# Kernel tuning notes

Measured on AMD Instinct MI355X. Metric: run time of the kernel, lower is better.

The kernel has to match this reference:

```python
import jax, jax.numpy as jnp
import numpy as np

B, N, D = 16, 4096, 128          # graphs, points per graph, feature dim
RATIO = 0.25
M = int(N * RATIO)               # 1024 sampled points per graph (static)
RADIUS = 0.2


def setup_inputs() -> dict:
    key = jax.random.key(0)
    k1, k2 = jax.random.split(key)
    x = jax.random.normal(k1, (B * N, D), dtype=jnp.float32)
    pos = jax.random.uniform(k2, (B * N, 3), dtype=jnp.float32)  # unit cube
    batch = jnp.repeat(jnp.arange(B, dtype=jnp.int32), N)        # sorted, equal-size graphs
    return {"x": x, "pos": pos, "batch": batch}


def _fps(pos_g):
    """Farthest point sampling on one graph. pos_g: [N,3] -> [M] int indices.
    Deterministic start at index 0 (random_start=False, i.e. eval mode)."""
    def step(carry, _):
        dist, last = carry
        d = jnp.sum((pos_g - pos_g[last]) ** 2, axis=-1)   # [N]
        dist = jnp.minimum(dist, d)                        # dist to nearest selected
        nxt = jnp.argmax(dist).astype(jnp.int32)
        return (dist, nxt), last
    init = (jnp.full((pos_g.shape[0],), jnp.inf, pos_g.dtype), jnp.int32(0))
    _, idx = jax.lax.scan(step, init, None, length=M)
    return idx  # [M]


def reference(x, pos, batch):
    # Equal-size graphs -> reshape instead of segment bookkeeping.
    pos_b = pos.reshape(B, N, 3)
    x_b = x.reshape(B, N, D)

    # FPS per graph, vmapped (sequential greedy selection inside lax.scan).
    idx = jax.vmap(_fps)(pos_b)                                    # [B, M]

    sampled_pos = jnp.take_along_axis(pos_b, idx[:, :, None], axis=1)  # [B, M, 3]
    sampled_x = jnp.take_along_axis(x_b, idx[:, :, None], axis=1)      # [B, M, D]

    # radius_graph within each graph: boolean adjacency (j within r of i, no self loops).
    diff = sampled_pos[:, :, None, :] - sampled_pos[:, None, :, :]     # [B, M, M, 3]
    d2 = jnp.sum(diff * diff, axis=-1)                                 # [B, M, M]
    adj = (d2 <= RADIUS * RADIUS) & ~jnp.eye(M, dtype=bool)[None]      # [B, M, M]

    sampled_batch = jnp.repeat(jnp.arange(B, dtype=batch.dtype), M)    # [B*M]
    return (sampled_x.reshape(B * M, D),
            sampled_pos.reshape(B * M, 3),
            sampled_batch,
            adj)
```

## Files before the change

kernel.cpp:

```cpp
#include <hip/hip_runtime.h>
#include <stdint.h>

#define BB 16
#define NN 4096
#define DD 128
#define MM 1024
#define RADIUS2 0.04f
#define TPB 256
#define PPT 16
#define NPAIR (PPT / 2)
#define NW 4

typedef unsigned long long u64;
typedef unsigned int u32;
typedef float f32x2 __attribute__((ext_vector_type(2)));
typedef unsigned int uint2v __attribute__((ext_vector_type(2)));

__device__ __forceinline__ u32 umin2(u32 a, u32 b) { return a < b ? a : b; }
__device__ __forceinline__ u32 umin3(u32 a, u32 b, u32 c) { return umin2(umin2(a, b), c); }
__device__ __forceinline__ float fmax3(float a, float b, float c) { return fmaxf(fmaxf(a, b), c); }

template <int CTRL>
__device__ __forceinline__ float dpp_fmax(float v) {
    int o = __builtin_amdgcn_update_dpp(0, __float_as_int(v), CTRL, 0xF, 0xF, true);
    return fmaxf(v, __int_as_float(o));
}
__device__ __forceinline__ float xor16_fmax(float v) {
#if __has_builtin(__builtin_amdgcn_permlane16_swap)
    uint2v r = __builtin_amdgcn_permlane16_swap(__float_as_uint(v), __float_as_uint(v), false, false);
    return fmaxf(__uint_as_float(r[0]), __uint_as_float(r[1]));
#else
    int o = __builtin_amdgcn_ds_swizzle(__float_as_int(v), 0x401F);
    return fmaxf(v, __int_as_float(o));
#endif
}
__device__ __forceinline__ float xor32_fmax(float v) {
#if __has_builtin(__builtin_amdgcn_permlane32_swap)
    uint2v r = __builtin_amdgcn_permlane32_swap(__float_as_uint(v), __float_as_uint(v), false, false);
    return fmaxf(__uint_as_float(r[0]), __uint_as_float(r[1]));
#else
    return fmaxf(v, __shfl_xor(v, 32, 64));
#endif
}
__device__ __forceinline__ float wave_fmax(float v) {
    v = dpp_fmax<0xB1>(v);
    v = dpp_fmax<0x4E>(v);
    v = dpp_fmax<0x141>(v);
    v = dpp_fmax<0x140>(v);
    v = xor16_fmax(v);
    v = xor32_fmax(v);
    return v;
}

__global__ __launch_bounds__(TPB) void fps_kernel(const float* __restrict__ pos,
                                                  int* __restrict__ idx_out) {
    const int b    = blockIdx.x;
    const int tid  = threadIdx.x;
    const int wid  = tid >> 6;
    const int lane = tid & 63;

    __shared__ float4 pos4[NN];
    __shared__ __align__(16) float4 cslot[2][NW];
    __shared__ __align__(16) u32    tslot[2][NW];
    __shared__ int trace[MM];

    const float* pg = pos + (size_t)b * NN * 3;
    for (int k = tid; k < NN * 3; k += TPB)
        ((float*)&pos4[k / 3])[k % 3] = pg[k];
    if (tid < 8) ((u32*)tslot)[tid] = 0;
    if (tid == 0) trace[0] = 0;
    __syncthreads();

    const int base = tid * PPT;
    f32x2 px[NPAIR], py[NPAIR], pz[NPAIR], dist2[NPAIR];
#pragma unroll
    for (int j = 0; j < NPAIR; ++j) {
        float4 a = pos4[base + 2 * j];
        float4 c = pos4[base + 2 * j + 1];
        px[j] = (f32x2){a.x, c.x};
        py[j] = (f32x2){a.y, c.y};
        pz[j] = (f32x2){a.z, c.z};
        dist2[j] = (f32x2){__builtin_inff(), __builtin_inff()};
    }

    float4 lp = pos4[0];
    float lx = lp.x, ly = lp.y, lz = lp.z;

    for (int m = 1; m < MM; ++m) {
        {
#pragma clang fp contract(off)
            f32x2 vx = {lx, lx}, vy = {ly, ly}, vz = {lz, lz};
#pragma unroll
            for (int j = 0; j < NPAIR; ++j) {
                f32x2 dx = px[j] - vx;
                f32x2 dy = py[j] - vy;
                f32x2 dz = pz[j] - vz;
                f32x2 d  = dx * dx + dy * dy;
                d = d + dz * dz;
                dist2[j] = __builtin_elementwise_min(dist2[j], d);
            }
        }

        float t0 = fmaxf(dist2[0].x, dist2[0].y);
        float t1 = fmaxf(dist2[1].x, dist2[1].y);
        float t2 = fmaxf(dist2[2].x, dist2[2].y);
        float t3 = fmaxf(dist2[3].x, dist2[3].y);
        float t4 = fmaxf(dist2[4].x, dist2[4].y);
        float t5 = fmaxf(dist2[5].x, dist2[5].y);
        float t6 = fmaxf(dist2[6].x, dist2[6].y);
        float t7 = fmaxf(dist2[7].x, dist2[7].y);
        float tmax = fmax3(fmax3(t0, t1, t2), fmax3(t3, t4, t5), fmaxf(t6, t7));

        u32 c[PPT];
#pragma unroll
        for (int j = 0; j < NPAIR; ++j) {
            c[2 * j]     = (dist2[j].x == tmax) ? (u32)(2 * j)     : 64u;
            c[2 * j + 1] = (dist2[j].y == tmax) ? (u32)(2 * j + 1) : 64u;
        }
        u32 a0 = umin3(c[0],  c[1],  c[2]);
        u32 a1 = umin3(c[3],  c[4],  c[5]);
        u32 a2 = umin3(c[6],  c[7],  c[8]);
        u32 a3 = umin3(c[9],  c[10], c[11]);
        u32 a4 = umin3(c[12], c[13], c[14]);
        u32 sl = umin3(umin3(a0, a1, a2), umin2(a3, a4), c[15]);
        u32 gidx = (u32)base + sl;

        float4 sp = pos4[gidx];

        float wmax = wave_fmax(tmax);

        u64 mk    = __ballot(tmax == wmax);
        int owner = (int)__builtin_ctzll(mk);

        const int buf = m & 1;
        const u32 tagm = (u32)m << 12;
        if (lane == owner) {
            cslot[buf][wid] = make_float4(sp.x, sp.y, sp.z, wmax);
            asm volatile("" ::: "memory");
            tslot[buf][wid] = tagm | gidx;
        }

        uint4 tg; float4 q0, q1, q2, q3;
        do {
            asm volatile("" ::: "memory");
            tg = *(const uint4*)&tslot[buf][0];
            q0 = cslot[buf][0];
            q1 = cslot[buf][1];
            q2 = cslot[buf][2];
            q3 = cslot[buf][3];
        } while ((((tg.x ^ tagm) | (tg.y ^ tagm) | (tg.z ^ tagm) | (tg.w ^ tagm))
                  & 0xFFFFF000u) != 0);

        float g = fmaxf(fmaxf(q0.w, q1.w), fmaxf(q2.w, q3.w));
        float nx = q3.x, ny = q3.y, nz = q3.z; u32 li = tg.w & 0xFFFu;
        bool s2 = (q2.w == g); nx = s2 ? q2.x : nx; ny = s2 ? q2.y : ny; nz = s2 ? q2.z : nz; li = s2 ? (tg.z & 0xFFFu) : li;
        bool s1 = (q1.w == g); nx = s1 ? q1.x : nx; ny = s1 ? q1.y : ny; nz = s1 ? q1.z : nz; li = s1 ? (tg.y & 0xFFFu) : li;
        bool s0 = (q0.w == g); nx = s0 ? q0.x : nx; ny = s0 ? q0.y : ny; nz = s0 ? q0.z : nz; li = s0 ? (tg.x & 0xFFFu) : li;
        lx = nx; ly = ny; lz = nz;

        if (tid == 0) trace[m] = (int)li;
    }

    __syncthreads();
    for (int k = tid; k < MM; k += TPB)
        idx_out[b * MM + k] = trace[k];
}

__global__ void gather_x_kernel(const float* __restrict__ x,
                                const int* __restrict__ idx,
                                float* __restrict__ out) {
    int t = blockIdx.x * blockDim.x + threadIdx.x;
    if (t >= BB * MM * DD / 4) return;
    int row = t >> 5;
    int c4  = (t & 31) << 2;
    int b   = row >> 10;
    int n   = idx[row];
    const float4 v = *(const float4*)(x + ((size_t)(b * NN + n) * DD + c4));
    *(float4*)(out + (size_t)row * DD + c4) = v;
}

__global__ void gather_pb_kernel(const float* __restrict__ pos,
                                 const int* __restrict__ idx,
                                 float* __restrict__ spos,
                                 float* __restrict__ sbatch) {
    int r = blockIdx.x * blockDim.x + threadIdx.x;
    if (r >= BB * MM) return;
    int b = r >> 10;
    int n = idx[r];
    const float* p = pos + (size_t)(b * NN + n) * 3;
    spos[r * 3 + 0] = p[0];
    spos[r * 3 + 1] = p[1];
    spos[r * 3 + 2] = p[2];
    sbatch[r] = (float)b;
}

__global__ void adj_kernel(const float* __restrict__ spos,
                           float* __restrict__ adj) {
    int row = blockIdx.x;
    int b   = row >> 10;
    int i   = row & (MM - 1);
    const float* pb = spos + (size_t)b * MM * 3;
    float xi = pb[i * 3 + 0];
    float yi = pb[i * 3 + 1];
    float zi = pb[i * 3 + 2];

    int j0 = threadIdx.x << 2;
    float4 r;
    float* o = adj + (size_t)row * MM;
#pragma unroll
    for (int k = 0; k < 4; ++k) {
        int j = j0 + k;
        float dx = xi - pb[j * 3 + 0];
        float dy = yi - pb[j * 3 + 1];
        float dz = zi - pb[j * 3 + 2];
        float d2 = __fadd_rn(__fadd_rn(__fmul_rn(dx, dx), __fmul_rn(dy, dy)),
                             __fmul_rn(dz, dz));
        float v = (d2 <= RADIUS2 && j != i) ? 1.0f : 0.0f;
        ((float*)&r)[k] = v;
    }
    *(float4*)(o + j0) = r;
}

extern "C" void kernel_launch(void* const* d_in, const int* in_sizes, int n_in,
                              void* d_out, int out_size, void* d_ws, size_t ws_size,
                              hipStream_t stream) {
    const float* x   = (const float*)d_in[0];
    const float* pos = (const float*)d_in[1];

    float* out    = (float*)d_out;
    int*   idx_ws = (int*)d_ws;

    float* sx   = out;
    float* spos = sx + (size_t)BB * MM * DD;
    float* sbat = spos + (size_t)BB * MM * 3;
    float* adj  = sbat + (size_t)BB * MM;

    fps_kernel<<<BB, TPB, 0, stream>>>(pos, idx_ws);
    gather_x_kernel<<<(BB * MM * DD / 4 + 255) / 256, 256, 0, stream>>>(x, idx_ws, sx);
    gather_pb_kernel<<<(BB * MM + 255) / 256, 256, 0, stream>>>(pos, idx_ws, spos, sbat);
    adj_kernel<<<BB * MM, 256, 0, stream>>>(spos, adj);
}
```

Baseline: 744.0 us.

## Process two graphs per FPS block and replace spin-wait with barrier

The FPS kernel now handles two graphs per workgroup, interleaving their distance updates and reductions so the independent dependency chains can hide each other's latency. It launches half as many blocks. The tag-polling spin loop on shared memory is replaced by a __syncthreads barrier per iteration. This doubles register use per thread and halves the number of concurrently active CUs, trading parallelism for instruction-level overlap.

```diff
diff --git a/kernel.cpp b/kernel.cpp
--- a/kernel.cpp
+++ b/kernel.cpp
@@ -54,116 +54,152 @@
 
 __global__ __launch_bounds__(TPB) void fps_kernel(const float* __restrict__ pos,
                                                   int* __restrict__ idx_out) {
-    const int b    = blockIdx.x;
     const int tid  = threadIdx.x;
     const int wid  = tid >> 6;
     const int lane = tid & 63;
-
-    __shared__ float4 pos4[NN];
-    __shared__ __align__(16) float4 cslot[2][NW];
-    __shared__ __align__(16) u32    tslot[2][NW];
-    __shared__ int trace[MM];
-
-    const float* pg = pos + (size_t)b * NN * 3;
-    for (int k = tid; k < NN * 3; k += TPB)
-        ((float*)&pos4[k / 3])[k % 3] = pg[k];
-    if (tid < 8) ((u32*)tslot)[tid] = 0;
-    if (tid == 0) trace[0] = 0;
+    const int gA   = blockIdx.x * 2;
+    const int gB   = gA + 1;
+
+    __shared__ float4 posA[NN], posB[NN];
+    __shared__ float4 fpart[2][2][NW];
+    __shared__ u32    ipart[2][2][NW];
+    __shared__ int    trace[2][MM];
+
+    const float* pga = pos + (size_t)gA * NN * 3;
+    const float* pgb = pos + (size_t)gB * NN * 3;
+    for (int k = tid; k < NN * 3; k += TPB) {
+        ((float*)&posA[k / 3])[k % 3] = pga[k];
+        ((float*)&posB[k / 3])[k % 3] = pgb[k];
+    }
+    if (tid == 0) { trace[0][0] = 0; trace[1][0] = 0; }
     __syncthreads();
 
     const int base = tid * PPT;
-    f32x2 px[NPAIR], py[NPAIR], pz[NPAIR], dist2[NPAIR];
+    f32x2 pxA[NPAIR], pyA[NPAIR], pzA[NPAIR], dA[NPAIR];
+    f32x2 pxB[NPAIR], pyB[NPAIR], pzB[NPAIR], dB[NPAIR];
 #pragma unroll
     for (int j = 0; j < NPAIR; ++j) {
-        float4 a = pos4[base + 2 * j];
-        float4 c = pos4[base + 2 * j + 1];
-        px[j] = (f32x2){a.x, c.x};
-        py[j] = (f32x2){a.y, c.y};
-        pz[j] = (f32x2){a.z, c.z};
-        dist2[j] = (f32x2){__builtin_inff(), __builtin_inff()};
-    }
-
-    float4 lp = pos4[0];
-    float lx = lp.x, ly = lp.y, lz = lp.z;
+        float4 a0 = posA[base + 2 * j], a1 = posA[base + 2 * j + 1];
+        pxA[j] = (f32x2){a0.x, a1.x}; pyA[j] = (f32x2){a0.y, a1.y}; pzA[j] = (f32x2){a0.z, a1.z};
+        dA[j] = (f32x2){__builtin_inff(), __builtin_inff()};
+        float4 b0 = posB[base + 2 * j], b1 = posB[base + 2 * j + 1];
+        pxB[j] = (f32x2){b0.x, b1.x}; pyB[j] = (f32x2){b0.y, b1.y}; pzB[j] = (f32x2){b0.z, b1.z};
+        dB[j] = (f32x2){__builtin_inff(), __builtin_inff()};
+    }
+
+    float4 lpA = posA[0], lpB = posB[0];
+    float lxa = lpA.x, lya = lpA.y, lza = lpA.z;
+    float lxb = lpB.x, lyb = lpB.y, lzb = lpB.z;
 
     for (int m = 1; m < MM; ++m) {
         {
 #pragma clang fp contract(off)
-            f32x2 vx = {lx, lx}, vy = {ly, ly}, vz = {lz, lz};
+            f32x2 vxa = {lxa, lxa}, vya = {lya, lya}, vza = {lza, lza};
+            f32x2 vxb = {lxb, lxb}, vyb = {lyb, lyb}, vzb = {lzb, lzb};
 #pragma unroll
             for (int j = 0; j < NPAIR; ++j) {
-                f32x2 dx = px[j] - vx;
-                f32x2 dy = py[j] - vy;
-                f32x2 dz = pz[j] - vz;
-                f32x2 d  = dx * dx + dy * dy;
-                d = d + dz * dz;
-                dist2[j] = __builtin_elementwise_min(dist2[j], d);
+                f32x2 dxa = pxA[j] - vxa, dya = pyA[j] - vya, dza = pzA[j] - vza;
+                f32x2 dxb = pxB[j] - vxb, dyb = pyB[j] - vyb, dzb = pzB[j] - vzb;
+                f32x2 da = dxa * dxa + dya * dya; da = da + dza * dza;
+                f32x2 db = dxb * dxb + dyb * dyb; db = db + dzb * dzb;
+                dA[j] = __builtin_elementwise_min(dA[j], da);
+                dB[j] = __builtin_elementwise_min(dB[j], db);
             }
         }
 
-        float t0 = fmaxf(dist2[0].x, dist2[0].y);
-        float t1 = fmaxf(dist2[1].x, dist2[1].y);
-        float t2 = fmaxf(dist2[2].x, dist2[2].y);
-        float t3 = fmaxf(dist2[3].x, dist2[3].y);
-        float t4 = fmaxf(dist2[4].x, dist2[4].y);
-        float t5 = fmaxf(dist2[5].x, dist2[5].y);
-        float t6 = fmaxf(dist2[6].x, dist2[6].y);
-        float t7 = fmaxf(dist2[7].x, dist2[7].y);
-        float tmax = fmax3(fmax3(t0, t1, t2), fmax3(t3, t4, t5), fmaxf(t6, t7));
-
-        u32 c[PPT];
+        float ta0 = fmaxf(dA[0].x, dA[0].y), ta1 = fmaxf(dA[1].x, dA[1].y);
+        float ta2 = fmaxf(dA[2].x, dA[2].y), ta3 = fmaxf(dA[3].x, dA[3].y);
+        float ta4 = fmaxf(dA[4].x, dA[4].y), ta5 = fmaxf(dA[5].x, dA[5].y);
+        float ta6 = fmaxf(dA[6].x, dA[6].y), ta7 = fmaxf(dA[7].x, dA[7].y);
+        float tmaxA = fmax3(fmax3(ta0, ta1, ta2), fmax3(ta3, ta4, ta5), fmaxf(ta6, ta7));
+        float tb0 = fmaxf(dB[0].x, dB[0].y), tb1 = fmaxf(dB[1].x, dB[1].y);
+        float tb2 = fmaxf(dB[2].x, dB[2].y), tb3 = fmaxf(dB[3].x, dB[3].y);
+        float tb4 = fmaxf(dB[4].x, dB[4].y), tb5 = fmaxf(dB[5].x, dB[5].y);
+        float tb6 = fmaxf(dB[6].x, dB[6].y), tb7 = fmaxf(dB[7].x, dB[7].y);
+        float tmaxB = fmax3(fmax3(tb0, tb1, tb2), fmax3(tb3, tb4, tb5), fmaxf(tb6, tb7));
+
+        u32 cA[PPT], cB[PPT];
 #pragma unroll
         for (int j = 0; j < NPAIR; ++j) {
-            c[2 * j]     = (dist2[j].x == tmax) ? (u32)(2 * j)     : 64u;
-            c[2 * j + 1] = (dist2[j].y == tmax) ? (u32)(2 * j + 1) : 64u;
-        }
-        u32 a0 = umin3(c[0],  c[1],  c[2]);
-        u32 a1 = umin3(c[3],  c[4],  c[5]);
-        u32 a2 = umin3(c[6],  c[7],  c[8]);
-        u32 a3 = umin3(c[9],  c[10], c[11]);
-        u32 a4 = umin3(c[12], c[13], c[14]);
-        u32 sl = umin3(umin3(a0, a1, a2), umin2(a3, a4), c[15]);
-        u32 gidx = (u32)base + sl;
-
-        float4 sp = pos4[gidx];
-
-        float wmax = wave_fmax(tmax);
-
-        u64 mk    = __ballot(tmax == wmax);
-        int owner = (int)__builtin_ctzll(mk);
+            cA[2 * j]     = (dA[j].x == tmaxA) ? (u32)(2 * j)     : 64u;
+            cA[2 * j + 1] = (dA[j].y == tmaxA) ? (u32)(2 * j + 1) : 64u;
+            cB[2 * j]     = (dB[j].x == tmaxB) ? (u32)(2 * j)     : 64u;
+            cB[2 * j + 1] = (dB[j].y == tmaxB) ? (u32)(2 * j + 1) : 64u;
+        }
+        u32 sA = umin3(umin3(umin3(cA[0], cA[1], cA[2]),  umin3(cA[3], cA[4], cA[5]),
+                             umin3(cA[6], cA[7], cA[8])),
+                       umin2(umin3(cA[9], cA[10], cA[11]), umin3(cA[12], cA[13], cA[14])),
+                       cA[15]);
+        u32 sB = umin3(umin3(umin3(cB[0], cB[1], cB[2]),  umin3(cB[3], cB[4], cB[5]),
+                             umin3(cB[6], cB[7], cB[8])),
+                       umin2(umin3(cB[9], cB[10], cB[11]), umin3(cB[12], cB[13], cB[14])),
+                       cB[15]);
+        u32 gidxA = (u32)base + sA;
+        u32 gidxB = (u32)base + sB;
+
+        float4 spA = posA[gidxA];
+        float4 spB = posB[gidxB];
+
+        float wmaxA = wave_fmax(tmaxA);
+        float wmaxB = wave_fmax(tmaxB);
+
+        u64 mkA = __ballot(tmaxA == wmaxA);
+        u64 mkB = __ballot(tmaxB == wmaxB);
+        int ownerA = (int)__builtin_ctzll(mkA);
+        int ownerB = (int)__builtin_ctzll(mkB);
 
         const int buf = m & 1;
-        const u32 tagm = (u32)m << 12;
-        if (lane == owner) {
-            cslot[buf][wid] = make_float4(sp.x, sp.y, sp.z, wmax);
-            asm volatile("" ::: "memory");
-            tslot[buf][wid] = tagm | gidx;
-        }
-
-        uint4 tg; float4 q0, q1, q2, q3;
-        do {
-            asm volatile("" ::: "memory");
-            tg = *(const uint4*)&tslot[buf][0];
-            q0 = cslot[buf][0];
-            q1 = cslot[buf][1];
-            q2 = cslot[buf][2];
-            q3 = cslot[buf][3];
-        } while ((((tg.x ^ tagm) | (tg.y ^ tagm) | (tg.z ^ tagm) | (tg.w ^ tagm))
-                  & 0xFFFFF000u) != 0);
-
-        float g = fmaxf(fmaxf(q0.w, q1.w), fmaxf(q2.w, q3.w));
-        float nx = q3.x, ny = q3.y, nz = q3.z; u32 li = tg.w & 0xFFFu;
-        bool s2 = (q2.w == g); nx = s2 ? q2.x : nx; ny = s2 ? q2.y : ny; nz = s2 ? q2.z : nz; li = s2 ? (tg.z & 0xFFFu) : li;
-        bool s1 = (q1.w == g); nx = s1 ? q1.x : nx; ny = s1 ? q1.y : ny; nz = s1 ? q1.z : nz; li = s1 ? (tg.y & 0xFFFu) : li;
-        bool s0 = (q0.w == g); nx = s0 ? q0.x : nx; ny = s0 ? q0.y : ny; nz = s0 ? q0.z : nz; li = s0 ? (tg.x & 0xFFFu) : li;
-        lx = nx; ly = ny; lz = nz;
-
-        if (tid == 0) trace[m] = (int)li;
+        if (lane == ownerA) {
+            fpart[0][buf][wid] = make_float4(wmaxA, spA.x, spA.y, spA.z);
+            ipart[0][buf][wid] = gidxA;
+        }
+        if (lane == ownerB) {
+            fpart[1][buf][wid] = make_float4(wmaxB, spB.x, spB.y, spB.z);
+            ipart[1][buf][wid] = gidxB;
+        }
+        __syncthreads();
+
+        {
+            float4 q0 = fpart[0][buf][0], q1 = fpart[0][buf][1];
+            float4 q2 = fpart[0][buf][2], q3 = fpart[0][buf][3];
+            float g = fmaxf(fmaxf(q0.x, q1.x), fmaxf(q2.x, q3.x));
+            float nx = q3.y, ny = q3.z, nz = q3.w;
+            bool s2 = (q2.x == g); nx = s2 ? q2.y : nx; ny = s2 ? q2.z : ny; nz = s2 ? q2.w : nz;
+            bool s1 = (q1.x == g); nx = s1 ? q1.y : nx; ny = s1 ? q1.z : ny; nz = s1 ? q1.w : nz;
+            bool s0 = (q0.x == g); nx = s0 ? q0.y : nx; ny = s0 ? q0.z : ny; nz = s0 ? q0.w : nz;
+            lxa = nx; lya = ny; lza = nz;
+            if (tid == 0) {
+                u32 li = ipart[0][buf][3];
+                li = s2 ? ipart[0][buf][2] : li;
+                li = s1 ? ipart[0][buf][1] : li;
+                li = s0 ? ipart[0][buf][0] : li;
+                trace[0][m] = (int)li;
+            }
+        }
+        {
+            float4 q0 = fpart[1][buf][0], q1 = fpart[1][buf][1];
+            float4 q2 = fpart[1][buf][2], q3 = fpart[1][buf][3];
+            float g = fmaxf(fmaxf(q0.x, q1.x), fmaxf(q2.x, q3.x));
+            float nx = q3.y, ny = q3.z, nz = q3.w;
+            bool s2 = (q2.x == g); nx = s2 ? q2.y : nx; ny = s2 ? q2.z : ny; nz = s2 ? q2.w : nz;
+            bool s1 = (q1.x == g); nx = s1 ? q1.y : nx; ny = s1 ? q1.z : ny; nz = s1 ? q1.w : nz;
+            bool s0 = (q0.x == g); nx = s0 ? q0.y : nx; ny = s0 ? q0.z : ny; nz = s0 ? q0.w : nz;
+            lxb = nx; lyb = ny; lzb = nz;
+            if (tid == 0) {
+                u32 li = ipart[1][buf][3];
+                li = s2 ? ipart[1][buf][2] : li;
+                li = s1 ? ipart[1][buf][1] : li;
+                li = s0 ? ipart[1][buf][0] : li;
+                trace[1][m] = (int)li;
+            }
+        }
     }
 
     __syncthreads();
-    for (int k = tid; k < MM; k += TPB)
-        idx_out[b * MM + k] = trace[k];
+    for (int k = tid; k < MM; k += TPB) {
+        idx_out[gA * MM + k] = trace[0][k];
+        idx_out[gB * MM + k] = trace[1][k];
+    }
 }
 
 __global__ void gather_x_kernel(const float* __restrict__ x,
@@ -235,7 +271,7 @@
     float* sbat = spos + (size_t)BB * MM * 3;
     float* adj  = sbat + (size_t)BB * MM;
 
-    fps_kernel<<<BB, TPB, 0, stream>>>(pos, idx_ws);
+    fps_kernel<<<BB / 2, TPB, 0, stream>>>(pos, idx_ws);
     gather_x_kernel<<<(BB * MM * DD / 4 + 255) / 256, 256, 0, stream>>>(x, idx_ws, sx);
     gather_pb_kernel<<<(BB * MM + 255) / 256, 256, 0, stream>>>(pos, idx_ws, spos, sbat);
     adj_kernel<<<BB * MM, 256, 0, stream>>>(spos, adj);
```

New measurement: 1.274 ms. 71.2% more time.
